# Kernel tuning notes

Measured on AMD Instinct MI355X. Metric: run time of the kernel, lower is better.

The kernel has to match this reference:

```python
import jax, jax.numpy as jnp
import numpy as np

B, P, M, W = 32, 4096, 12, 9
IN_C, OUT_C = 64, 64
IN_PN_PAD = P + 1  # in_point_num + 1 padding row


def setup_inputs() -> dict:
    key = jax.random.key(0)
    k1, k2, k3, k4 = jax.random.split(key, 4)
    in_pc_pad = jax.random.normal(k1, (B, IN_PN_PAD, IN_C), dtype=jnp.float32)
    weights = jax.random.normal(k2, (W, OUT_C * IN_C), dtype=jnp.float32)
    bias = jnp.zeros((OUT_C,), dtype=jnp.float32)
    w_weights = jax.random.normal(k3, (P, M, W), dtype=jnp.float32) / (9.0 * W)
    neighbor_id_lstlst = jax.random.randint(k4, (P, M), 0, IN_PN_PAD, dtype=jnp.int64)
    neighbor_mask_lst = jnp.ones((P, M), dtype=jnp.float32)
    return {
        "in_pc_pad": in_pc_pad,
        "weights": weights,
        "bias": bias,
        "w_weights": w_weights,
        "neighbor_id_lstlst": neighbor_id_lstlst,
        "neighbor_mask_lst": neighbor_mask_lst,
    }


def reference(in_pc_pad, weights, bias, w_weights, neighbor_id_lstlst, neighbor_mask_lst):
    # gather neighbor features: [B, P, M, IN_C]
    in_neighbors = in_pc_pad[:, neighbor_id_lstlst]
    # mask the per-(point,neighbor) basis coefficients: [P, M, W]
    w2 = w_weights * neighbor_mask_lst[:, :, None]
    # synthesize per-(point,neighbor) weight matrices from basis: [P, M, OUT_C, IN_C]
    wmat = jnp.einsum('pmw,wc->pmc', w2, weights).reshape(P, M, OUT_C, IN_C)
    # batched matvec + neighbor-sum reduce (fused over m): [B, P, OUT_C]
    out_pc = jnp.einsum('pmoi,bpmi->bpo', wmat, in_neighbors)
    return out_pc + bias
```

## Files before the change

### kernel.cpp

```cpp
#include <hip/hip_runtime.h>
#include <hip/hip_bf16.h>

#define NB 32
#define NP 4096
#define NM 12
#define NW 9
#define NC 64
#define PN_PAD 4097
#define KDIM (NW * NC)
#define KSTEPS (KDIM / 32)
#define AROW 584

#define WSW_BYTES (KDIM * NC * 2)
#define W2_OFFSET WSW_BYTES

typedef __attribute__((ext_vector_type(8))) short short8;
typedef __attribute__((ext_vector_type(4))) float float4v;

__device__ __forceinline__ unsigned short f32_to_bf16(float f) {
    union { float f; unsigned u; } v; v.f = f;
    unsigned r = v.u + 0x7FFFu + ((v.u >> 16) & 1u);
    return (unsigned short)(r >> 16);
}

__device__ __forceinline__ uint2 pack_bf16x4(float4v v) {
    union { float f; unsigned u; } a0, a1, a2, a3;
    a0.f = v[0]; a1.f = v[1]; a2.f = v[2]; a3.f = v[3];
    unsigned u0 = a0.u + 0x8000u, u1 = a1.u + 0x8000u;
    unsigned u2 = a2.u + 0x8000u, u3 = a3.u + 0x8000u;
    uint2 r;
    r.x = __builtin_amdgcn_perm(u1, u0, 0x07060302u);
    r.y = __builtin_amdgcn_perm(u3, u2, 0x07060302u);
    return r;
}

__global__ void prep(const float* __restrict__ w,
                     const float* __restrict__ ww,
                     const float* __restrict__ mask,
                     unsigned short* __restrict__ wsw,
                     float* __restrict__ w2d) {
    int idx = blockIdx.x * 256 + threadIdx.x;
    if (idx < KDIM * NC) {
        int j    = idx & 7;
        int lane = (idx >> 3) & 63;
        int nt   = (idx >> 9) & 3;
        int ks   = idx >> 11;
        int k = ks * 32 + ((lane >> 4) * 8) + j;
        int n = nt * 16 + (lane & 15);
        int wi = k >> 6;
        int ii = k & 63;
        wsw[idx] = f32_to_bf16(w[wi * (NC * NC) + n * NC + ii]);
    }
    if (idx < NP * NM * NW) {
        int wq = idx % NW;
        int pm = idx / NW;
        w2d[pm * 12 + wq] = ww[idx] * mask[pm];
    }
}

__global__ __launch_bounds__(256)
void conv_main(const float* __restrict__ x,
               const unsigned short* __restrict__ wsw,
               const float* __restrict__ bias,
               const float* __restrict__ w2d,
               const int* __restrict__ nid,
               float* __restrict__ out)
{
    __shared__ __align__(16) unsigned short A[NB * AROW];

    const int p = blockIdx.x;
    const int tid = threadIdx.x;

    {
        const int i4 = tid & 15;
        const int bs = tid >> 4;
        const float4v* x4 = (const float4v*)x;
        const float* w2p = w2d + p * (NM * 12);
        const int* nidp = nid + p * NM;

        int nm[NM];
        #pragma unroll
        for (int m = 0; m < NM; ++m) nm[m] = nidp[m];

        float4v acc0[NW], acc1[NW];
        #pragma unroll
        for (int w = 0; w < NW; ++w) {
            acc0[w] = (float4v){0.f, 0.f, 0.f, 0.f};
            acc1[w] = (float4v){0.f, 0.f, 0.f, 0.f};
        }

        #pragma unroll 2
        for (int m = 0; m < NM; ++m) {
            const float4v xv0 = x4[(bs * PN_PAD + nm[m]) * 16 + i4];
            const float4v xv1 = x4[((bs + 16) * PN_PAD + nm[m]) * 16 + i4];
            #pragma unroll
            for (int w = 0; w < NW; ++w) {
                const float wv = w2p[m * 12 + w];
                acc0[w] += wv * xv0;
                acc1[w] += wv * xv1;
            }
        }

        #pragma unroll
        for (int w = 0; w < NW; ++w) {
            *(uint2*)&A[bs * AROW + w * 64 + i4 * 4] = pack_bf16x4(acc0[w]);
            *(uint2*)&A[(bs + 16) * AROW + w * 64 + i4 * 4] = pack_bf16x4(acc1[w]);
        }
    }
    __syncthreads();

    {
        const int lane = tid & 63;
        const int nt   = tid >> 6;
        const int quad = lane >> 4;
        const int l15  = lane & 15;

        float4v acc0 = {0.f, 0.f, 0.f, 0.f};
        float4v acc1 = {0.f, 0.f, 0.f, 0.f};
        const short8* Bfrags = (const short8*)wsw;

        #pragma unroll
        for (int ks = 0; ks < KSTEPS; ++ks) {
            short8 bfrag = Bfrags[(ks * 4 + nt) * 64 + lane];
            const short8 a0 = *(const short8*)&A[(l15     ) * AROW + ks * 32 + quad * 8];
            const short8 a1 = *(const short8*)&A[(16 + l15) * AROW + ks * 32 + quad * 8];
            acc0 = __builtin_amdgcn_mfma_f32_16x16x32_bf16(a0, bfrag, acc0, 0, 0, 0);
            acc1 = __builtin_amdgcn_mfma_f32_16x16x32_bf16(a1, bfrag, acc1, 0, 0, 0);
        }

        const int o = nt * 16 + l15;
        const float bv = bias[o];
        #pragma unroll
        for (int reg = 0; reg < 4; ++reg) {
            const int r0 = quad * 4 + reg;
            out[(r0 * NP + p) * NC + o] = acc0[reg] + bv;
            const int r1 = 16 + r0;
            out[(r1 * NP + p) * NC + o] = acc1[reg] + bv;
        }
    }
}

extern "C" void kernel_launch(void* const* d_in, const int* in_sizes, int n_in,
                              void* d_out, int out_size, void* d_ws, size_t ws_size,
                              hipStream_t stream) {
    const float* x    = (const float*)d_in[0];
    const float* w    = (const float*)d_in[1];
    const float* bias = (const float*)d_in[2];
    const float* ww   = (const float*)d_in[3];
    const int*   nid  = (const int*)d_in[4];
    const float* mask = (const float*)d_in[5];
    float* out = (float*)d_out;
    unsigned short* wsw = (unsigned short*)d_ws;
    float* w2d = (float*)((char*)d_ws + W2_OFFSET);

    const int prep_elems = NP * NM * NW;
    hipLaunchKernelGGL(prep, dim3((prep_elems + 255) / 256), dim3(256), 0, stream,
                       w, ww, mask, wsw, w2d);
    hipLaunchKernelGGL(conv_main, dim3(NP), dim3(256), 0, stream,
                       x, wsw, bias, w2d, nid, out);
}
```

Measured before the change: 144.9 us.

## Double block threads so each thread handles one batch and one MFMA tile

Raises conv_main to 512 threads per block. Each thread now gathers neighbors for a single batch row, issuing all 12 neighbor loads up front, instead of covering two batch rows. Each wave computes one 16x16 output tile instead of two. The goal is more memory-level parallelism for the scattered gather and shorter per-thread dependency chains. The cost is fewer blocks resident per CU, B-fragment loads duplicated across the two M-tile waves, and more registers per thread for the hoisted loads.

Result: no change. 142.6 us (-1.6%).

```diff
diff --git a/kernel.cpp b/kernel.cpp
--- a/kernel.cpp
+++ b/kernel.cpp
@@ -58,7 +58,7 @@
     }
 }
 
-__global__ __launch_bounds__(256)
+__global__ __launch_bounds__(512)
 void conv_main(const float* __restrict__ x,
                const unsigned short* __restrict__ wsw,
                const float* __restrict__ bias,
@@ -73,7 +73,7 @@
 
     {
         const int i4 = tid & 15;
-        const int bs = tid >> 4;
+        const int b  = tid >> 4;
         const float4v* x4 = (const float4v*)x;
         const float* w2p = w2d + p * (NM * 12);
         const int* nidp = nid + p * NM;
@@ -82,60 +82,63 @@
         #pragma unroll
         for (int m = 0; m < NM; ++m) nm[m] = nidp[m];
 
-        float4v acc0[NW], acc1[NW];
+        float4v acc[NW];
         #pragma unroll
-        for (int w = 0; w < NW; ++w) {
-            acc0[w] = (float4v){0.f, 0.f, 0.f, 0.f};
-            acc1[w] = (float4v){0.f, 0.f, 0.f, 0.f};
+        for (int w = 0; w < NW; ++w) acc[w] = (float4v){0.f, 0.f, 0.f, 0.f};
+
+        float4v xv0[6];
+        #pragma unroll
+        for (int m = 0; m < 6; ++m)
+            xv0[m] = x4[(b * PN_PAD + nm[m]) * 16 + i4];
+        float4v xv1[6];
+        #pragma unroll
+        for (int m = 0; m < 6; ++m)
+            xv1[m] = x4[(b * PN_PAD + nm[6 + m]) * 16 + i4];
+
+        #pragma unroll
+        for (int m = 0; m < 6; ++m) {
+            #pragma unroll
+            for (int w = 0; w < NW; ++w)
+                acc[w] += w2p[m * 12 + w] * xv0[m];
         }
-
-        #pragma unroll 2
-        for (int m = 0; m < NM; ++m) {
-            const float4v xv0 = x4[(bs * PN_PAD + nm[m]) * 16 + i4];
-            const float4v xv1 = x4[((bs + 16) * PN_PAD + nm[m]) * 16 + i4];
+        #pragma unroll
+        for (int m = 0; m < 6; ++m) {
             #pragma unroll
-            for (int w = 0; w < NW; ++w) {
-                const float wv = w2p[m * 12 + w];
-                acc0[w] += wv * xv0;
-                acc1[w] += wv * xv1;
-            }
+            for (int w = 0; w < NW; ++w)
+                acc[w] += w2p[(6 + m) * 12 + w] * xv1[m];
         }
 
         #pragma unroll
-        for (int w = 0; w < NW; ++w) {
-            *(uint2*)&A[bs * AROW + w * 64 + i4 * 4] = pack_bf16x4(acc0[w]);
-            *(uint2*)&A[(bs + 16) * AROW + w * 64 + i4 * 4] = pack_bf16x4(acc1[w]);
-        }
+        for (int w = 0; w < NW; ++w)
+            *(uint2*)&A[b * AROW + w * 64 + i4 * 4] = pack_bf16x4(acc[w]);
     }
     __syncthreads();
 
     {
         const int lane = tid & 63;
-        const int nt   = tid >> 6;
+        const int wid  = tid >> 6;
+        const int nt   = wid & 3;
+        const int mt   = wid >> 2;
         const int quad = lane >> 4;
         const int l15  = lane & 15;
 
-        float4v acc0 = {0.f, 0.f, 0.f, 0.f};
-        float4v acc1 = {0.f, 0.f, 0.f, 0.f};
+        float4v acc = {0.f, 0.f, 0.f, 0.f};
         const short8* Bfrags = (const short8*)wsw;
+        const int arow = mt * 16 + l15;
 
         #pragma unroll
         for (int ks = 0; ks < KSTEPS; ++ks) {
             short8 bfrag = Bfrags[(ks * 4 + nt) * 64 + lane];
-            const short8 a0 = *(const short8*)&A[(l15     ) * AROW + ks * 32 + quad * 8];
-            const short8 a1 = *(const short8*)&A[(16 + l15) * AROW + ks * 32 + quad * 8];
-            acc0 = __builtin_amdgcn_mfma_f32_16x16x32_bf16(a0, bfrag, acc0, 0, 0, 0);
-            acc1 = __builtin_amdgcn_mfma_f32_16x16x32_bf16(a1, bfrag, acc1, 0, 0, 0);
+            const short8 a = *(const short8*)&A[arow * AROW + ks * 32 + quad * 8];
+            acc = __builtin_amdgcn_mfma_f32_16x16x32_bf16(a, bfrag, acc, 0, 0, 0);
         }
 
         const int o = nt * 16 + l15;
         const float bv = bias[o];
         #pragma unroll
         for (int reg = 0; reg < 4; ++reg) {
-            const int r0 = quad * 4 + reg;
-            out[(r0 * NP + p) * NC + o] = acc0[reg] + bv;
-            const int r1 = 16 + r0;
-            out[(r1 * NP + p) * NC + o] = acc1[reg] + bv;
+            const int b = mt * 16 + quad * 4 + reg;
+            out[(b * NP + p) * NC + o] = acc[reg] + bv;
         }
     }
 }
@@ -156,6 +159,6 @@
     const int prep_elems = NP * NM * NW;
     hipLaunchKernelGGL(prep, dim3((prep_elems + 255) / 256), dim3(256), 0, stream,
                        w, ww, mask, wsw, w2d);
-    hipLaunchKernelGGL(conv_main, dim3(NP), dim3(256), 0, stream,
+    hipLaunchKernelGGL(conv_main, dim3(NP), dim3(512), 0, stream,
                        x, wsw, bias, w2d, nid, out);
 }
```
